# Performance work log

Measured on AMD Instinct MI355X. Metric: run time of the kernel, lower is better.

The kernel has to match this reference:

```python
import jax, jax.numpy as jnp
import numpy as np

EMB_DIM = 512
NUM_HEADS = 8
HEAD_DIM = EMB_DIM // NUM_HEADS


def setup_inputs() -> dict:
    key = jax.random.key(0)
    ks = jax.random.split(key, 8)
    B, S, D = 2, 192, EMB_DIM
    return {
        "q": jax.random.normal(ks[0], (B, S, D), dtype=jnp.float32),
        "k": jax.random.normal(ks[1], (B, S, D), dtype=jnp.float32),
        "l": jax.random.normal(ks[2], (B, S, D), dtype=jnp.float32),
        "v": jax.random.normal(ks[3], (B, S, D), dtype=jnp.float32),
        "Wq": jax.random.normal(ks[4], (D, D), dtype=jnp.float32) * (1.0 / np.sqrt(D)),
        "Wk": jax.random.normal(ks[5], (D, D), dtype=jnp.float32) * (1.0 / np.sqrt(D)),
        "Wv": jax.random.normal(ks[6], (D, D), dtype=jnp.float32) * (1.0 / np.sqrt(D)),
        "Wout": jax.random.normal(ks[7], (D, D), dtype=jnp.float32) * (1.0 / np.sqrt(D)),
    }


def _heads(x, W):
    # torch nn.Linear: x @ W.T ; then split heads -> (B, H, S, hd)
    B, S, D = x.shape
    y = x @ W.T
    return y.reshape(B, S, NUM_HEADS, HEAD_DIM).transpose(0, 2, 1, 3)


def reference(q, k, l, v, Wq, Wk, Wv, Wout):
    B, QS, D = q.shape
    KS, LS = k.shape[1], l.shape[1]
    qh = _heads(q, Wq)
    kh = _heads(k, Wk)
    lh = _heads(l, Wk)  # NOTE: original module projects l with self.key (faithful)
    vh = _heads(v, Wv)
    # rank-3 attention scores: (B, H, QS, KS, LS)
    scores = jnp.einsum('bhqe,bhke,bhle->bhqkl', qh, kh, lh) / jnp.sqrt(
        jnp.asarray(HEAD_DIM, dtype=q.dtype))
    # softmax jointly over (KS, LS)
    attn = jax.nn.softmax(scores.reshape(B, NUM_HEADS, QS, KS * LS), axis=-1)
    attn = attn.reshape(B, NUM_HEADS, QS, KS, LS)
    # vv[b,h,l,k,d] = v[b,h,k,d]; contract over k and l -> (B, QS, H, hd)
    attended = jnp.einsum('bhqkl,bhkd->bqhd', attn, vh)
    concatenated = attended.reshape(B, QS, EMB_DIM)
    return concatenated @ Wout.T
```

## Files before the change

### kernel.cpp

```cpp
#include <hip/hip_runtime.h>
#include <math.h>

#define BB 2
#define SS 192
#define DD 512
#define HH 8
#define HD 64
#define QCB 6
#define NQC (SS / QCB)
#define PROJ_N (BB*HH*SS*HD)
#define SCL (0.125f * 1.44269504088896f)

typedef __attribute__((ext_vector_type(8))) short bf16x8;
typedef __attribute__((ext_vector_type(4))) float f32x4;
typedef __attribute__((ext_vector_type(4))) unsigned uint4v;
typedef _Float16 f16x8 __attribute__((ext_vector_type(8)));

__device__ __forceinline__ f16x8 cvt8_f16_rne(const float* g) {
    f16x8 r;
#pragma unroll
    for (int i = 0; i < 8; ++i) r[i] = (_Float16)g[i];
    return r;
}

template <int SPLIT>
__device__ __forceinline__ void gemm_mfma_body(const float* __restrict__ x,
                                               const float* __restrict__ W,
                                               float* __restrict__ y) {
    __shared__ short Ahs[2][4 * 64 * 8];
    __shared__ short Bhs[2][4 * 64 * 8];

    const int t = threadIdx.x;
    const int lane = t & 63, w = t >> 6;
    const int wr = w >> 1, wc = w & 1;
    const int c16 = lane & 15, q4 = lane >> 4;
    const int m0 = blockIdx.x * 64, n0 = blockIdx.y * 64;
    const int sr = t >> 2, scc = t & 3;

    f32x4 acc[2][2];
#pragma unroll
    for (int a = 0; a < 2; ++a)
#pragma unroll
        for (int b = 0; b < 2; ++b) acc[a][b] = (f32x4){0.f, 0.f, 0.f, 0.f};

#define STAGE(kk, bf)                                                              \
    {                                                                              \
        float a8[8], w8[8];                                                        \
        *(f32x4*)&a8[0] = *(const f32x4*)&x[(m0 + sr) * 512 + (kk) + scc * 8];     \
        *(f32x4*)&a8[4] = *(const f32x4*)&x[(m0 + sr) * 512 + (kk) + scc * 8 + 4]; \
        *(f32x4*)&w8[0] = *(const f32x4*)&W[(n0 + sr) * 512 + (kk) + scc * 8];     \
        *(f32x4*)&w8[4] = *(const f32x4*)&W[(n0 + sr) * 512 + (kk) + scc * 8 + 4]; \
        *(f16x8*)&Ahs[bf][(scc * 64 + sr) * 8] = cvt8_f16_rne(a8);                 \
        *(f16x8*)&Bhs[bf][(scc * 64 + sr) * 8] = cvt8_f16_rne(w8);                 \
    }

    STAGE(0, 0)
    for (int s = 0; s < 16; ++s) {
        __syncthreads();
        if (s + 1 < 16) STAGE((s + 1) * 32, (s + 1) & 1)
        const int b = s & 1;
        f16x8 aH[2], bH[2];
#pragma unroll
        for (int mt = 0; mt < 2; ++mt) {
            const int row = wr * 32 + mt * 16 + c16;
            aH[mt] = *(const f16x8*)&Ahs[b][(q4 * 64 + row) * 8];
        }
#pragma unroll
        for (int nt = 0; nt < 2; ++nt) {
            const int col = wc * 32 + nt * 16 + c16;
            bH[nt] = *(const f16x8*)&Bhs[b][(q4 * 64 + col) * 8];
        }
#pragma unroll
        for (int mt = 0; mt < 2; ++mt)
#pragma unroll
            for (int nt = 0; nt < 2; ++nt)
                acc[mt][nt] = __builtin_amdgcn_mfma_f32_16x16x32_f16(aH[mt], bH[nt], acc[mt][nt], 0, 0, 0);
    }
#undef STAGE

#pragma unroll
    for (int mt = 0; mt < 2; ++mt)
#pragma unroll
        for (int nt = 0; nt < 2; ++nt)
#pragma unroll
            for (int j = 0; j < 4; ++j) {
                const int n_row = m0 + wr * 32 + mt * 16 + q4 * 4 + j;
                const int col = n0 + wc * 32 + nt * 16 + c16;
                const float v = acc[mt][nt][j];
                if (SPLIT) {
                    const int b = n_row / SS, s2 = n_row % SS;
                    const int h = col >> 6, e = col & 63;
                    y[((b * HH + h) * SS + s2) * HD + e] = v;
                } else {
                    y[n_row * 512 + col] = v;
                }
            }
}

__global__ __launch_bounds__(256) void proj4_kernel(
    const float* __restrict__ xq, const float* __restrict__ xk,
    const float* __restrict__ xl, const float* __restrict__ xv,
    const float* __restrict__ Wq, const float* __restrict__ Wk,
    const float* __restrict__ Wv, float* __restrict__ ws) {
    const int p = blockIdx.z;
    const float* x = (p == 0) ? xq : (p == 1) ? xk : (p == 2) ? xl : xv;
    const float* W = (p == 0) ? Wq : (p == 3) ? Wv : Wk;
    gemm_mfma_body<1>(x, W, ws + p * PROJ_N);
}

__global__ __launch_bounds__(256) void outproj_kernel(
    const float* __restrict__ att, const float* __restrict__ Wout,
    float* __restrict__ out) {
    gemm_mfma_body<0>(att, Wout, out);
}

__global__ __launch_bounds__(512, 4) void attn3d_mfma_kernel(
    const float* __restrict__ qh, const float* __restrict__ kh,
    const float* __restrict__ lh, const float* __restrict__ vh,
    float* __restrict__ att) {
    __shared__ short Kf16[8][193][8];
    __shared__ short Lf16[8][193][8];
    __shared__ short qpk[QCB][8][8];
    __shared__ float partial[2][QCB][196];
    __shared__ float Wt[QCB][192];
    __shared__ float zinv[QCB];

    const int blk = blockIdx.x;
    const int bh = blk >> 5, qc = blk & 31;
    const int t = threadIdx.x;
    const int lane = t & 63, w = t >> 6;
    const int lg = w >> 2, kg = w & 3;
    const int c = lane & 15, eh = lane >> 4;

    if (t < QCB * 64) {
        const int q = t >> 6, e = t & 63;
        const float v = qh[(bh * SS + qc * QCB + q) * HD + e] * SCL;
        qpk[q][e >> 3][e & 7] = __builtin_bit_cast(short, (_Float16)v);
    }
#pragma unroll
    for (int j = 0; j < 3; ++j) {
        const int cid = t + 512 * j;
        const int k = cid >> 3, ec = cid & 7;
        float b8[8];
        const float* kp = &kh[(bh * SS + k) * HD + ec * 8];
        *(f32x4*)&b8[0] = *(const f32x4*)&kp[0];
        *(f32x4*)&b8[4] = *(const f32x4*)&kp[4];
        *(f16x8*)&Kf16[ec][k][0] = cvt8_f16_rne(b8);
        const float* lp = &lh[(bh * SS + k) * HD + ec * 8];
        *(f32x4*)&b8[0] = *(const f32x4*)&lp[0];
        *(f32x4*)&b8[4] = *(const f32x4*)&lp[4];
        *(f16x8*)&Lf16[ec][k][0] = cvt8_f16_rne(b8);
    }
    __syncthreads();

    for (int q = 0; q < QCB; ++q) {
        const f16x8 qf0 = *(const f16x8*)&qpk[q][eh][0];
        const f16x8 qf1 = *(const f16x8*)&qpk[q][4 + eh][0];
        f16x8 Bf[3][2];
#pragma unroll
        for (int kt = 0; kt < 3; ++kt) {
            const int col = kg * 48 + kt * 16 + c;
            Bf[kt][0] = *(const f16x8*)&Kf16[eh][col][0] * qf0;
            Bf[kt][1] = *(const f16x8*)&Kf16[4 + eh][col][0] * qf1;
        }
        float rr0 = 0.f, rr1 = 0.f, rr2 = 0.f;
#pragma unroll
        for (int lt = 0; lt < 6; ++lt) {
            const int row = lg * 96 + lt * 16 + c;
            const f16x8 A0 = *(const f16x8*)&Lf16[eh][row][0];
            const f16x8 A1 = *(const f16x8*)&Lf16[4 + eh][row][0];
            f32x4 a0 = (f32x4){0.f, 0.f, 0.f, 0.f};
            f32x4 a1 = (f32x4){0.f, 0.f, 0.f, 0.f};
            f32x4 a2 = (f32x4){0.f, 0.f, 0.f, 0.f};
            a0 = __builtin_amdgcn_mfma_f32_16x16x32_f16(A0, Bf[0][0], a0, 0, 0, 0);
            a1 = __builtin_amdgcn_mfma_f32_16x16x32_f16(A0, Bf[1][0], a1, 0, 0, 0);
            a2 = __builtin_amdgcn_mfma_f32_16x16x32_f16(A0, Bf[2][0], a2, 0, 0, 0);
            a0 = __builtin_amdgcn_mfma_f32_16x16x32_f16(A1, Bf[0][1], a0, 0, 0, 0);
            a1 = __builtin_amdgcn_mfma_f32_16x16x32_f16(A1, Bf[1][1], a1, 0, 0, 0);
            a2 = __builtin_amdgcn_mfma_f32_16x16x32_f16(A1, Bf[2][1], a2, 0, 0, 0);
            rr0 += (__builtin_amdgcn_exp2f(a0[0]) + __builtin_amdgcn_exp2f(a0[1])) +
                   (__builtin_amdgcn_exp2f(a0[2]) + __builtin_amdgcn_exp2f(a0[3]));
            rr1 += (__builtin_amdgcn_exp2f(a1[0]) + __builtin_amdgcn_exp2f(a1[1])) +
                   (__builtin_amdgcn_exp2f(a1[2]) + __builtin_amdgcn_exp2f(a1[3]));
            rr2 += (__builtin_amdgcn_exp2f(a2[0]) + __builtin_amdgcn_exp2f(a2[1])) +
                   (__builtin_amdgcn_exp2f(a2[2]) + __builtin_amdgcn_exp2f(a2[3]));
        }
        rr0 += __shfl_xor(rr0, 16, 64);
        rr1 += __shfl_xor(rr1, 16, 64);
        rr2 += __shfl_xor(rr2, 16, 64);
        rr0 += __shfl_xor(rr0, 32, 64);
        rr1 += __shfl_xor(rr1, 32, 64);
        rr2 += __shfl_xor(rr2, 32, 64);
        if (eh == 0) {
            partial[lg][q][kg * 48 + 0 * 16 + c] = rr0;
            partial[lg][q][kg * 48 + 1 * 16 + c] = rr1;
            partial[lg][q][kg * 48 + 2 * 16 + c] = rr2;
        }
    }
    __syncthreads();

    for (int id = t; id < QCB * 192; id += 512) {
        const int q = id / 192, k = id - q * 192;
        Wt[q][k] = partial[0][q][k] + partial[1][q][k];
    }
    __syncthreads();

    if (w < QCB) {
        const int q = w;
        float z = Wt[q][lane] + Wt[q][lane + 64] + Wt[q][lane + 128];
#pragma unroll
        for (int off = 32; off >= 1; off >>= 1) z += __shfl_xor(z, off, 64);
        if (lane == 0) zinv[q] = 1.f / z;
    }
    __syncthreads();

    const int b = bh >> 3, h = bh & 7;
    if (t < QCB * 64) {
        const int q = t >> 6, d = t & 63;
        const float* vp = vh + bh * SS * HD + d;
        float sum = 0.f;
        for (int k0 = 0; k0 < SS; k0 += 8) {
            float v8[8];
#pragma unroll
            for (int j = 0; j < 8; ++j) v8[j] = vp[(k0 + j) * HD];
#pragma unroll
            for (int j = 0; j < 8; ++j) sum = fmaf(Wt[q][k0 + j], v8[j], sum);
        }
        att[(b * SS + qc * QCB + q) * DD + h * HD + d] = sum * zinv[q];
    }
}

extern "C" void kernel_launch(void* const* d_in, const int* in_sizes, int n_in,
                              void* d_out, int out_size, void* d_ws, size_t ws_size,
                              hipStream_t stream) {
    (void)in_sizes; (void)n_in; (void)out_size; (void)ws_size;
    const float* q    = (const float*)d_in[0];
    const float* k    = (const float*)d_in[1];
    const float* l    = (const float*)d_in[2];
    const float* v    = (const float*)d_in[3];
    const float* Wq   = (const float*)d_in[4];
    const float* Wk   = (const float*)d_in[5];
    const float* Wv   = (const float*)d_in[6];
    const float* Wout = (const float*)d_in[7];
    float* out = (float*)d_out;

    float* ws  = (float*)d_ws;
    float* qhp = ws + 0 * PROJ_N;
    float* khp = ws + 1 * PROJ_N;
    float* lhp = ws + 2 * PROJ_N;
    float* vhp = ws + 3 * PROJ_N;
    float* atp = ws + 4 * PROJ_N;

    proj4_kernel<<<dim3(384 / 64, 512 / 64, 4), 256, 0, stream>>>(
        q, k, l, v, Wq, Wk, Wv, ws);
    attn3d_mfma_kernel<<<dim3(16 * NQC), 512, 0, stream>>>(qhp, khp, lhp, vhp, atp);
    outproj_kernel<<<dim3(384 / 64, 512 / 64), 256, 0, stream>>>(atp, Wout, out);
}
```

Before: 50.04 us.

## Double GEMM K-tile depth and keep L fragments in registers in attention

The projection GEMM now stages 64-wide K slices instead of 32, halving the number of barrier-separated iterations and issuing two MFMAs per accumulator per stage. The attention kernel drops the shared-memory L tile and loads each wave's L fragments directly from global into registers once, reused across all query rows. This cuts LDS traffic, shared-memory footprint and synchronisation count, at the cost of more registers (12 f16x8 held live) and higher LDS use in the GEMM, which may reduce occupancy.

```diff
diff --git a/kernel.cpp b/kernel.cpp
--- a/kernel.cpp
+++ b/kernel.cpp
@@ -11,9 +11,7 @@
 #define PROJ_N (BB*HH*SS*HD)
 #define SCL (0.125f * 1.44269504088896f)
 
-typedef __attribute__((ext_vector_type(8))) short bf16x8;
 typedef __attribute__((ext_vector_type(4))) float f32x4;
-typedef __attribute__((ext_vector_type(4))) unsigned uint4v;
 typedef _Float16 f16x8 __attribute__((ext_vector_type(8)));
 
 __device__ __forceinline__ f16x8 cvt8_f16_rne(const float* g) {
@@ -27,15 +25,15 @@
 __device__ __forceinline__ void gemm_mfma_body(const float* __restrict__ x,
                                                const float* __restrict__ W,
                                                float* __restrict__ y) {
-    __shared__ short Ahs[2][4 * 64 * 8];
-    __shared__ short Bhs[2][4 * 64 * 8];
+    __shared__ short Ahs[2][8 * 64 * 8];
+    __shared__ short Bhs[2][8 * 64 * 8];
 
     const int t = threadIdx.x;
     const int lane = t & 63, w = t >> 6;
     const int wr = w >> 1, wc = w & 1;
     const int c16 = lane & 15, q4 = lane >> 4;
     const int m0 = blockIdx.x * 64, n0 = blockIdx.y * 64;
-    const int sr = t >> 2, scc = t & 3;
+    const int r = t >> 2, cc = t & 3;
 
     f32x4 acc[2][2];
 #pragma unroll
@@ -43,38 +41,45 @@
 #pragma unroll
         for (int b = 0; b < 2; ++b) acc[a][b] = (f32x4){0.f, 0.f, 0.f, 0.f};
 
-#define STAGE(kk, bf)                                                              \
-    {                                                                              \
-        float a8[8], w8[8];                                                        \
-        *(f32x4*)&a8[0] = *(const f32x4*)&x[(m0 + sr) * 512 + (kk) + scc * 8];     \
-        *(f32x4*)&a8[4] = *(const f32x4*)&x[(m0 + sr) * 512 + (kk) + scc * 8 + 4]; \
-        *(f32x4*)&w8[0] = *(const f32x4*)&W[(n0 + sr) * 512 + (kk) + scc * 8];     \
-        *(f32x4*)&w8[4] = *(const f32x4*)&W[(n0 + sr) * 512 + (kk) + scc * 8 + 4]; \
-        *(f16x8*)&Ahs[bf][(scc * 64 + sr) * 8] = cvt8_f16_rne(a8);                 \
-        *(f16x8*)&Bhs[bf][(scc * 64 + sr) * 8] = cvt8_f16_rne(w8);                 \
+#define STAGE(kk, bf)                                                               \
+    {                                                                               \
+        _Pragma("unroll") for (int h2 = 0; h2 < 2; ++h2) {                          \
+            const int ec = cc * 2 + h2;                                             \
+            float a8[8], w8[8];                                                     \
+            *(f32x4*)&a8[0] = *(const f32x4*)&x[(m0 + r) * 512 + (kk) + ec * 8];    \
+            *(f32x4*)&a8[4] = *(const f32x4*)&x[(m0 + r) * 512 + (kk) + ec * 8 + 4];\
+            *(f32x4*)&w8[0] = *(const f32x4*)&W[(n0 + r) * 512 + (kk) + ec * 8];    \
+            *(f32x4*)&w8[4] = *(const f32x4*)&W[(n0 + r) * 512 + (kk) + ec * 8 + 4];\
+            *(f16x8*)&Ahs[bf][(ec * 64 + r) * 8] = cvt8_f16_rne(a8);                \
+            *(f16x8*)&Bhs[bf][(ec * 64 + r) * 8] = cvt8_f16_rne(w8);                \
+        }                                                                           \
     }
 
     STAGE(0, 0)
-    for (int s = 0; s < 16; ++s) {
+    for (int s = 0; s < 8; ++s) {
         __syncthreads();
-        if (s + 1 < 16) STAGE((s + 1) * 32, (s + 1) & 1)
+        if (s + 1 < 8) STAGE((s + 1) * 64, (s + 1) & 1)
         const int b = s & 1;
-        f16x8 aH[2], bH[2];
+        f16x8 aH[2][2], bH[2][2];
 #pragma unroll
         for (int mt = 0; mt < 2; ++mt) {
             const int row = wr * 32 + mt * 16 + c16;
-            aH[mt] = *(const f16x8*)&Ahs[b][(q4 * 64 + row) * 8];
+            aH[mt][0] = *(const f16x8*)&Ahs[b][(q4 * 64 + row) * 8];
+            aH[mt][1] = *(const f16x8*)&Ahs[b][((q4 + 4) * 64 + row) * 8];
         }
 #pragma unroll
         for (int nt = 0; nt < 2; ++nt) {
             const int col = wc * 32 + nt * 16 + c16;
-            bH[nt] = *(const f16x8*)&Bhs[b][(q4 * 64 + col) * 8];
+            bH[nt][0] = *(const f16x8*)&Bhs[b][(q4 * 64 + col) * 8];
+            bH[nt][1] = *(const f16x8*)&Bhs[b][((q4 + 4) * 64 + col) * 8];
         }
 #pragma unroll
         for (int mt = 0; mt < 2; ++mt)
 #pragma unroll
-            for (int nt = 0; nt < 2; ++nt)
-                acc[mt][nt] = __builtin_amdgcn_mfma_f32_16x16x32_f16(aH[mt], bH[nt], acc[mt][nt], 0, 0, 0);
+            for (int nt = 0; nt < 2; ++nt) {
+                acc[mt][nt] = __builtin_amdgcn_mfma_f32_16x16x32_f16(aH[mt][0], bH[nt][0], acc[mt][nt], 0, 0, 0);
+                acc[mt][nt] = __builtin_amdgcn_mfma_f32_16x16x32_f16(aH[mt][1], bH[nt][1], acc[mt][nt], 0, 0, 0);
+            }
     }
 #undef STAGE
 
@@ -119,7 +124,6 @@
     const float* __restrict__ lh, const float* __restrict__ vh,
     float* __restrict__ att) {
     __shared__ short Kf16[8][193][8];
-    __shared__ short Lf16[8][193][8];
     __shared__ short qpk[QCB][8][8];
     __shared__ float partial[2][QCB][196];
     __shared__ float Wt[QCB][192];
@@ -146,11 +150,19 @@
         *(f32x4*)&b8[0] = *(const f32x4*)&kp[0];
         *(f32x4*)&b8[4] = *(const f32x4*)&kp[4];
         *(f16x8*)&Kf16[ec][k][0] = cvt8_f16_rne(b8);
-        const float* lp = &lh[(bh * SS + k) * HD + ec * 8];
-        *(f32x4*)&b8[0] = *(const f32x4*)&lp[0];
-        *(f32x4*)&b8[4] = *(const f32x4*)&lp[4];
-        *(f16x8*)&Lf16[ec][k][0] = cvt8_f16_rne(b8);
-    }
+    }
+    f16x8 Af[6][2];
+#pragma unroll
+    for (int lt = 0; lt < 6; ++lt)
+#pragma unroll
+        for (int s = 0; s < 2; ++s) {
+            const int row = lg * 96 + lt * 16 + c;
+            float b8[8];
+            const float* lp = &lh[(bh * SS + row) * HD + s * 32 + eh * 8];
+            *(f32x4*)&b8[0] = *(const f32x4*)&lp[0];
+            *(f32x4*)&b8[4] = *(const f32x4*)&lp[4];
+            Af[lt][s] = cvt8_f16_rne(b8);
+        }
     __syncthreads();
 
     for (int q = 0; q < QCB; ++q) {
@@ -166,18 +178,15 @@
         float rr0 = 0.f, rr1 = 0.f, rr2 = 0.f;
 #pragma unroll
         for (int lt = 0; lt < 6; ++lt) {
-            const int row = lg * 96 + lt * 16 + c;
-            const f16x8 A0 = *(const f16x8*)&Lf16[eh][row][0];
-            const f16x8 A1 = *(const f16x8*)&Lf16[4 + eh][row][0];
             f32x4 a0 = (f32x4){0.f, 0.f, 0.f, 0.f};
             f32x4 a1 = (f32x4){0.f, 0.f, 0.f, 0.f};
             f32x4 a2 = (f32x4){0.f, 0.f, 0.f, 0.f};
-            a0 = __builtin_amdgcn_mfma_f32_16x16x32_f16(A0, Bf[0][0], a0, 0, 0, 0);
-            a1 = __builtin_amdgcn_mfma_f32_16x16x32_f16(A0, Bf[1][0], a1, 0, 0, 0);
-            a2 = __builtin_amdgcn_mfma_f32_16x16x32_f16(A0, Bf[2][0], a2, 0, 0, 0);
-            a0 = __builtin_amdgcn_mfma_f32_16x16x32_f16(A1, Bf[0][1], a0, 0, 0, 0);
-            a1 = __builtin_amdgcn_mfma_f32_16x16x32_f16(A1, Bf[1][1], a1, 0, 0, 0);
-            a2 = __builtin_amdgcn_mfma_f32_16x16x32_f16(A1, Bf[2][1], a2, 0, 0, 0);
+            a0 = __builtin_amdgcn_mfma_f32_16x16x32_f16(Af[lt][0], Bf[0][0], a0, 0, 0, 0);
+            a1 = __builtin_amdgcn_mfma_f32_16x16x32_f16(Af[lt][0], Bf[1][0], a1, 0, 0, 0);
+            a2 = __builtin_amdgcn_mfma_f32_16x16x32_f16(Af[lt][0], Bf[2][0], a2, 0, 0, 0);
+            a0 = __builtin_amdgcn_mfma_f32_16x16x32_f16(Af[lt][1], Bf[0][1], a0, 0, 0, 0);
+            a1 = __builtin_amdgcn_mfma_f32_16x16x32_f16(Af[lt][1], Bf[1][1], a1, 0, 0, 0);
+            a2 = __builtin_amdgcn_mfma_f32_16x16x32_f16(Af[lt][1], Bf[2][1], a2, 0, 0, 0);
             rr0 += (__builtin_amdgcn_exp2f(a0[0]) + __builtin_amdgcn_exp2f(a0[1])) +
                    (__builtin_amdgcn_exp2f(a0[2]) + __builtin_amdgcn_exp2f(a0[3]));
             rr1 += (__builtin_amdgcn_exp2f(a1[0]) + __builtin_amdgcn_exp2f(a1[1])) +
```

Result: slower. 52.14 us (+4.2%).
